# Kernel tuning notes

Hardware: AMD Instinct MI355X
Metric: run time of the kernel (lower is better)

The kernel has to match this reference:

```python
import jax, jax.numpy as jnp
import numpy as np

B, T, E, V, L, BLK = 2, 2048, 1024, 32000, 12, 2048


def setup_inputs() -> dict:
    key = jax.random.key(0)
    ks = jax.random.split(key, 10)
    std = 0.005  # FHE-friendly tiny init, matches nn.init.normal_(std=0.005)
    init = lambda k, shape: jax.random.normal(k, shape, jnp.float32) * std
    return {
        "idx": jax.random.randint(ks[0], (B, T), 0, V, dtype=jnp.int32),
        "wte": init(ks[1], (V, E)),
        "wpe": init(ks[2], (BLK, E)),
        "ln1_w": jnp.ones((L, E), jnp.float32),   # FHELayerNorm weights init to ones
        "Wq": init(ks[3], (L, E, E)),
        "Wk": init(ks[4], (L, E, E)),
        "Wv": init(ks[5], (L, E, E)),
        "Wo": init(ks[6], (L, E, E)),
        "ln2_w": jnp.ones((L, E), jnp.float32),
        "fc1": init(ks[7], (L, 2 * E, E)),
        "fc2": init(ks[8], (L, E, 2 * E)),
        "lnf_w": jnp.ones((E,), jnp.float32),
        "lm_head": init(ks[9], (V, E)),
    }


def reference(idx, wte, wpe, ln1_w, Wq, Wk, Wv, Wo, ln2_w, fc1, fc2, lnf_w, lm_head):
    t = idx.shape[1]
    # embeddings, each scaled by 0.01
    x = wte[idx] * 0.01 + (wpe[:t] * 0.01)[None, :, :]  # [B,T,E]

    n_layer = ln1_w.shape[0]
    # inter-block rescale: 0.1 after every block except the last
    scales = jnp.where(jnp.arange(n_layer) < n_layer - 1, 0.1, 1.0).astype(x.dtype)

    def block(x, p):
        ln1, wq, wk, wv, wo, ln2, f1, f2, s = p
        # FHELayerNorm: pure scaling
        h = x * ln1 * 0.1
        # attention (single head over full E, softmax-free quadratic weights)
        q = jnp.einsum('bte,fe->btf', h, wq) * 0.01
        k = jnp.einsum('bte,fe->btf', h, wk) * 0.01
        v = jnp.einsum('bte,fe->btf', h, wv) * 0.1
        a = jnp.einsum('btf,bsf->bts', q, k) * 0.01      # [B,T,T]
        a = a * a * 0.1 + a * 0.1                         # pointwise quadratic
        ao = jnp.einsum('bts,bsf->btf', a, v) * 0.01
        attn_out = jnp.einsum('btf,ef->bte', ao, wo) * 0.1
        x = (x * 0.5 + attn_out * 0.5) * 0.1
        # MLP with polynomial activation
        h2 = x * ln2 * 0.1
        m = jnp.einsum('bte,fe->btf', h2, f1) * 0.05      # [B,T,2E]
        m = m * m * 0.1 + m * 0.1
        m = jnp.einsum('btf,ef->bte', m, f2) * 0.05
        x = (x * 0.5 + m * 0.5) * 0.1
        return x * s, None

    x, _ = jax.lax.scan(block, x, (ln1_w, Wq, Wk, Wv, Wo, ln2_w, fc1, fc2, scales))
    x = x * lnf_w * 0.1  # final FHELayerNorm
    logits = jnp.einsum('bte,ve->btv', x, lm_head) * 0.5
    return logits
```

## Files before the change

kernel.cpp:

```cpp
#include <hip/hip_runtime.h>
#include <hip/hip_fp8.h>
#include <stdint.h>
#include <math.h>

typedef unsigned short u16;
typedef __attribute__((ext_vector_type(4))) short s16x4;
typedef __attribute__((ext_vector_type(4))) float f32x4;
typedef __attribute__((ext_vector_type(2))) long long llx2;

typedef __attribute__((address_space(1))) const uint32_t gas_u32;
typedef __attribute__((address_space(3))) uint32_t las_u32;

__device__ __forceinline__ u16 f2b(float f) {
  union { float f; uint32_t u; } v; v.f = f;
  uint32_t r = v.u + 0x7FFFu + ((v.u >> 16) & 1u);
  return (u16)(r >> 16);
}
__device__ __forceinline__ float b2f(u16 b) {
  union { uint32_t u; float f; } v; v.u = ((uint32_t)b) << 16; return v.f;
}
__device__ __forceinline__ uint8_t f8(float x) {
  __hip_fp8_e4m3 t(x);
  return (uint8_t)t.__x;
}
__device__ __forceinline__ int ipos(int k) {
  return (k & ~63) | (k & 7) | ((k & 32) >> 2) | ((k & 24) << 1);
}

__device__ __forceinline__ void gl_lds16(const void* g, void* l) {
  __builtin_amdgcn_global_load_lds((gas_u32*)g, (las_u32*)l, 16, 0, 0);
}
__device__ __forceinline__ void barrier_raw() {
  asm volatile("" ::: "memory");
  __builtin_amdgcn_s_barrier();
  asm volatile("" ::: "memory");
}

#define MM8(A_, B_, C_) __builtin_amdgcn_mfma_f32_16x16x32_fp8_fp8(A_, B_, C_, 0, 0, 0)

#define PHASE_MID() do { \
  asm volatile("s_waitcnt lgkmcnt(0)" ::: "memory"); \
  __builtin_amdgcn_sched_barrier(0); \
  __builtin_amdgcn_s_setprio(1); \
} while (0)
#define PHASE_END() do { \
  __builtin_amdgcn_s_setprio(0); \
  __builtin_amdgcn_sched_barrier(0); \
  barrier_raw(); \
} while (0)

__device__ __forceinline__ void xcd_swz(int nwg, int orig, int gx, int& bx, int& by) {
  const int xcd = orig & 7, rem = orig >> 3;
  const int qq = nwg >> 3, rr = nwg & 7;
  const int wg = (xcd < rr ? xcd * (qq + 1) : rr * (qq + 1) + (xcd - rr) * qq) + rem;
  bx = wg % gx; by = wg / gx;
}

struct GP8 {
  const uint8_t* A; long long asb;
  const uint8_t* B[3]; long long bsb;
  uint8_t* O[3]; long long osb;
  int K, lda, ldb, ldo;
  float m1[3], m2[3];
  int epi[3];
  int nsel, msel, nfirst;
  float qc;
  u16* xres; const float* lnw; float rscale; float oscale;
  uint8_t* h8out;
  float* fout; int ldf;
};

#define EPI_FRAG() do { \
  if (epi == 0) { \
    _Pragma("unroll") \
    for (int r = 0; r < 4; ++r) { \
      float y = (v[r] * m1v) * m2v; \
      Op[(size_t)(rbase + r) * p.ldo + ipos(col)] = f8(y); \
    } \
  } else if (epi == 1) { \
    const int b = rbase >> 11, rb = rbase & 2047; \
    uint32_t pk = 0; \
    _Pragma("unroll") \
    for (int r = 0; r < 4; ++r) { \
      float y = (v[r] * m1v) * m2v; \
      pk |= (uint32_t)f8(y) << (8 * r); \
    } \
    *(uint32_t*)(Op + (size_t)b * 2097152 + (size_t)col * 2048 + ipos(rb)) = pk; \
  } else if (epi == 2) { \
    _Pragma("unroll") \
    for (int r = 0; r < 4; ++r) { \
      float u = (v[r] * m1v) * m2v; \
      Op[(size_t)(rbase + r) * p.ldo + ipos(col)] = f8(u * u * p.qc + u); \
    } \
  } else if (epi == 3) { \
    _Pragma("unroll") \
    for (int r = 0; r < 4; ++r) { \
      float add = (v[r] * m1v) * m2v; \
      size_t ix = (size_t)(rbase + r) * 1024 + col; \
      float xn = (b2f(p.xres[ix]) + add) * p.rscale; \
      p.xres[ix] = f2b(xn); \
      float hv = xn * p.lnw[col] * 0.1f; \
      p.h8out[(size_t)(rbase + r) * 1024 + ipos(col)] = f8(hv * p.oscale); \
    } \
  } else { \
    _Pragma("unroll") \
    for (int r = 0; r < 4; ++r) \
      __builtin_nontemporal_store((v[r] * m1v) * m2v, \
                                  &p.fout[(size_t)(rbase + r) * p.ldf + col]); \
  } \
} while (0)

#define S8A(q, kh, t) do { \
  gl_lds16(gA0 + (size_t)(t) * 128 + (kh) * 64, lAw + (q) * 32768 + (kh) * 8192); \
  gl_lds16(gA1 + (size_t)(t) * 128 + (kh) * 64, lAw + (q) * 32768 + (kh) * 8192 + 4096); \
} while (0)
#define S8B(q, kh, t) do { \
  gl_lds16(gB0 + (size_t)(t) * 128 + (kh) * 64, lBw + (q) * 32768 + (kh) * 8192); \
  gl_lds16(gB1 + (size_t)(t) * 128 + (kh) * 64, lBw + (q) * 32768 + (kh) * 8192 + 4096); \
} while (0)

#define MF8() do { \
  acc[0][0]=MM8(a0[0],b0[0],acc[0][0]); acc[0][0]=MM8(a0[1],b0[1],acc[0][0]); \
  acc[0][1]=MM8(a0[0],b1[0],acc[0][1]); acc[0][1]=MM8(a0[1],b1[1],acc[0][1]); \
  acc[0][2]=MM8(a0[0],b2[0],acc[0][2]); acc[0][2]=MM8(a0[1],b2[1],acc[0][2]); \
  acc[0][3]=MM8(a0[0],b3[0],acc[0][3]); acc[0][3]=MM8(a0[1],b3[1],acc[0][3]); \
  acc[1][0]=MM8(a1[0],b0[0],acc[1][0]); acc[1][0]=MM8(a1[1],b0[1],acc[1][0]); \
  acc[1][1]=MM8(a1[0],b1[0],acc[1][1]); acc[1][1]=MM8(a1[1],b1[1],acc[1][1]); \
  acc[1][2]=MM8(a1[0],b2[0],acc[1][2]); acc[1][2]=MM8(a1[1],b2[1],acc[1][2]); \
  acc[1][3]=MM8(a1[0],b3[0],acc[1][3]); acc[1][3]=MM8(a1[1],b3[1],acc[1][3]); \
  acc[2][0]=MM8(a2[0],b0[0],acc[2][0]); acc[2][0]=MM8(a2[1],b0[1],acc[2][0]); \
  acc[2][1]=MM8(a2[0],b1[0],acc[2][1]); acc[2][1]=MM8(a2[1],b1[1],acc[2][1]); \
  acc[2][2]=MM8(a2[0],b2[0],acc[2][2]); acc[2][2]=MM8(a2[1],b2[1],acc[2][2]); \
  acc[2][3]=MM8(a2[0],b3[0],acc[2][3]); acc[2][3]=MM8(a2[1],b3[1],acc[2][3]); \
  acc[3][0]=MM8(a3[0],b0[0],acc[3][0]); acc[3][0]=MM8(a3[1],b0[1],acc[3][0]); \
  acc[3][1]=MM8(a3[0],b1[0],acc[3][1]); acc[3][1]=MM8(a3[1],b1[1],acc[3][1]); \
  acc[3][2]=MM8(a3[0],b2[0],acc[3][2]); acc[3][2]=MM8(a3[1],b2[1],acc[3][2]); \
  acc[3][3]=MM8(a3[0],b3[0],acc[3][3]); acc[3][3]=MM8(a3[1],b3[1],acc[3][3]); \
} while (0)

__global__ __launch_bounds__(256, 2) void gemm8_k(GP8 p) {
  extern __shared__ __attribute__((aligned(16))) char lds[];
  const int z = blockIdx.z;
  int bx, by;
  xcd_swz(gridDim.x * gridDim.y, blockIdx.y * gridDim.x + blockIdx.x, gridDim.x, bx, by);
  const int m0 = p.nfirst ? by * 128 : bx * 128;
  const int n0 = p.nfirst ? bx * 128 : by * 128;
  const int zi = p.nsel ? (n0 >> 10) : 0;
  const int nB = p.nsel ? (n0 & 1023) : n0;
  const uint8_t* __restrict__ Ap = p.A + (size_t)z * p.asb;
  const uint8_t* __restrict__ Bp = p.B[zi] + (size_t)(p.msel ? (m0 >> 11) : z) * p.bsb;

  const int tid = threadIdx.x, wid = tid >> 6, lane = tid & 63;
  const int wm = wid >> 1, wn = wid & 1;
  const int l15 = lane & 15, l4 = lane >> 4;
  const int cswz16 = (l4 ^ ((l15 >> 1) & 3)) * 16;

  const f32x4 vzero = {0.f, 0.f, 0.f, 0.f};
  f32x4 acc[4][4];
#pragma unroll
  for (int i = 0; i < 4; ++i)
#pragma unroll
    for (int j = 0; j < 4; ++j) acc[i][j] = vzero;

  const int sr = lane >> 2;
  const int cgB = ((lane & 3) ^ ((lane >> 3) & 3)) * 16;
  const uint8_t* gA0 = Ap + (size_t)(m0 + wid * 16 + sr) * p.lda + cgB;
  const uint8_t* gA1 = gA0 + (size_t)64 * p.lda;
  const uint8_t* gB0 = Bp + (size_t)(nB + wid * 16 + sr) * p.ldb + cgB;
  const uint8_t* gB1 = gB0 + (size_t)64 * p.ldb;
  char* lAw = lds + wid * 1024;
  char* lBw = lds + 16384 + wid * 1024;

  const int nt = p.K >> 7;

  S8A(0, 0, 0); S8B(0, 0, 0); S8A(0, 1, 0); S8B(0, 1, 0);
  S8A(1, 0, 1); S8B(1, 0, 1);
  asm volatile("s_waitcnt vmcnt(4)" ::: "memory");
  barrier_raw();

  llx2 a0, a1, a2, a3, b0, b1, b2, b3;
  for (int t = 0; t < nt; ++t) {
    const int q = t & 1;
    const char* Abase = lds + q * 32768 + (wm * 64 + l15) * 64 + cswz16;
    const char* Bbase = lds + q * 32768 + 16384 + (wn * 64 + l15) * 64 + cswz16;
    a0 = *(const llx2*)Abase;          a1 = *(const llx2*)(Abase + 1024);
    a2 = *(const llx2*)(Abase + 2048); a3 = *(const llx2*)(Abase + 3072);
    b0 = *(const llx2*)Bbase;          b1 = *(const llx2*)(Bbase + 1024);
    b2 = *(const llx2*)(Bbase + 2048); b3 = *(const llx2*)(Bbase + 3072);
    if (t + 1 < nt) { S8A(q ^ 1, 1, t + 1); S8B(q ^ 1, 1, t + 1); }
    PHASE_MID(); MF8(); PHASE_END();
    a0 = *(const llx2*)(Abase + 8192);        a1 = *(const llx2*)(Abase + 8192 + 1024);
    a2 = *(const llx2*)(Abase + 8192 + 2048); a3 = *(const llx2*)(Abase + 8192 + 3072);
    b0 = *(const llx2*)(Bbase + 8192);        b1 = *(const llx2*)(Bbase + 8192 + 1024);
    b2 = *(const llx2*)(Bbase + 8192 + 2048); b3 = *(const llx2*)(Bbase + 8192 + 3072);
    if (t + 2 < nt) { S8A(q, 0, t + 2); S8B(q, 0, t + 2); }
    PHASE_MID(); MF8();
    __builtin_amdgcn_s_setprio(0);
    __builtin_amdgcn_sched_barrier(0);
    if (t + 2 < nt) asm volatile("s_waitcnt vmcnt(4)" ::: "memory");
    else            asm volatile("s_waitcnt vmcnt(0)" ::: "memory");
    barrier_raw();
  }

  const int epi = p.epi[zi];
  const float m1v = p.m1[zi], m2v = p.m2[zi];
  uint8_t* __restrict__ Op = p.O[zi] + (size_t)z * p.osb;
#pragma unroll
  for (int mi = 0; mi < 4; ++mi) {
    const int rbase = m0 + wm * 64 + mi * 16 + l4 * 4;
#pragma unroll
    for (int ni = 0; ni < 4; ++ni) {
      const int col = nB + wn * 64 + ni * 16 + l15;
      f32x4 v = acc[mi][ni];
      EPI_FRAG();
    }
  }
}

#define H8STAGE(b, t) do { \
  gl_lds16(gA0 + (size_t)(t) * 128,      lds + (b) * 24576 + wid * 1024); \
  gl_lds16(gB0 + (size_t)(t) * 128,      lds + (b) * 24576 + 8192 + wid * 1024); \
  gl_lds16(gB1 + (size_t)(t) * 128,      lds + (b) * 24576 + 12288 + wid * 1024); \
  gl_lds16(gA0 + (size_t)(t) * 128 + 64, lds + (b) * 24576 + 4096 + wid * 1024); \
  gl_lds16(gB0 + (size_t)(t) * 128 + 64, lds + (b) * 24576 + 16384 + wid * 1024); \
  gl_lds16(gB1 + (size_t)(t) * 128 + 64, lds + (b) * 24576 + 20480 + wid * 1024); \
} while (0)

#define MF8H(AK, BK_) do { \
  acc[0][0]=MM8(a0##AK[0],b0##BK_[0],acc[0][0]); acc[0][0]=MM8(a0##AK[1],b0##BK_[1],acc[0][0]); \
  acc[0][1]=MM8(a0##AK[0],b1##BK_[0],acc[0][1]); acc[0][1]=MM8(a0##AK[1],b1##BK_[1],acc[0][1]); \
  acc[0][2]=MM8(a0##AK[0],b2##BK_[0],acc[0][2]); acc[0][2]=MM8(a0##AK[1],b2##BK_[1],acc[0][2]); \
  acc[0][3]=MM8(a0##AK[0],b3##BK_[0],acc[0][3]); acc[0][3]=MM8(a0##AK[1],b3##BK_[1],acc[0][3]); \
  acc[1][0]=MM8(a1##AK[0],b0##BK_[0],acc[1][0]); acc[1][0]=MM8(a1##AK[1],b0##BK_[1],acc[1][0]); \
  acc[1][1]=MM8(a1##AK[0],b1##BK_[0],acc[1][1]); acc[1][1]=MM8(a1##AK[1],b1##BK_[1],acc[1][1]); \
  acc[1][2]=MM8(a1##AK[0],b2##BK_[0],acc[1][2]); acc[1][2]=MM8(a1##AK[1],b2##BK_[1],acc[1][2]); \
  acc[1][3]=MM8(a1##AK[0],b3##BK_[0],acc[1][3]); acc[1][3]=MM8(a1##AK[1],b3##BK_[1],acc[1][3]); \
} while (0)

__global__ __launch_bounds__(256, 2) void gemm8h_k(GP8 p) {
  extern __shared__ __attribute__((aligned(16))) char lds[];
  const int z = blockIdx.z;
  int bx, by;
  xcd_swz(gridDim.x * gridDim.y, blockIdx.y * gridDim.x + blockIdx.x, gridDim.x, bx, by);
  const int m0 = bx * 64, n0 = by * 128;
  const int zi = p.nsel ? (n0 >> 10) : 0;
  const int nB = p.nsel ? (n0 & 1023) : n0;
  const uint8_t* __restrict__ Ap = p.A + (size_t)z * p.asb;
  const uint8_t* __restrict__ Bp = p.B[zi] + (size_t)(p.msel ? (m0 >> 11) : z) * p.bsb;

  const int tid = threadIdx.x, wid = tid >> 6, lane = tid & 63;
  const int wm = wid >> 1, wn = wid & 1;
  const int l15 = lane & 15, l4 = lane >> 4;
  const int cswz16 = (l4 ^ ((l15 >> 1) & 3)) * 16;

  const f32x4 vzero = {0.f, 0.f, 0.f, 0.f};
  f32x4 acc[2][4];
#pragma unroll
  for (int i = 0; i < 2; ++i)
#pragma unroll
    for (int j = 0; j < 4; ++j) acc[i][j] = vzero;

  const int sr = lane >> 2;
  const int cgB = ((lane & 3) ^ ((lane >> 3) & 3)) * 16;
  const uint8_t* gA0 = Ap + (size_t)(m0 + wid * 16 + sr) * p.lda + cgB;
  const uint8_t* gB0 = Bp + (size_t)(nB + wid * 16 + sr) * p.ldb + cgB;
  const uint8_t* gB1 = gB0 + (size_t)64 * p.ldb;

  const int nt = p.K >> 7;

  H8STAGE(0, 0);
  H8STAGE(1, 1);
  asm volatile("s_waitcnt vmcnt(6)" ::: "memory");
  barrier_raw();

  int q = 0;
  for (int t = 0; t < nt; ++t) {
    const int bn = (q == 0) ? 2 : q - 1;
    const char* Abase = lds + q * 24576 + (wm * 32 + l15) * 64 + cswz16;
    const char* Bbase = lds + q * 24576 + 8192 + (wn * 64 + l15) * 64 + cswz16;
    llx2 a0k0 = *(const llx2*)Abase;
    llx2 a1k0 = *(const llx2*)(Abase + 1024);
    llx2 a0k1 = *(const llx2*)(Abase + 4096);
    llx2 a1k1 = *(const llx2*)(Abase + 4096 + 1024);
    llx2 b0k0 = *(const llx2*)Bbase;
    llx2 b1k0 = *(const llx2*)(Bbase + 1024);
    llx2 b2k0 = *(const llx2*)(Bbase + 2048);
    llx2 b3k0 = *(const llx2*)(Bbase + 3072);
    llx2 b0k1 = *(const llx2*)(Bbase + 8192);
    llx2 b1k1 = *(const llx2*)(Bbase + 8192 + 1024);
    llx2 b2k1 = *(const llx2*)(Bbase + 8192 + 2048);
    llx2 b3k1 = *(const llx2*)(Bbase + 8192 + 3072);
    if (t + 2 < nt) H8STAGE(bn, t + 2);
    asm volatile("s_waitcnt lgkmcnt(0)" ::: "memory");
    __builtin_amdgcn_sched_barrier(0);
    __builtin_amdgcn_s_setprio(1);
    MF8H(k0, k0);
    MF8H(k1, k1);
    __builtin_amdgcn_s_setprio(0);
    __builtin_amdgcn_sched_barrier(0);
    if (t + 2 < nt) asm volatile("s_waitcnt vmcnt(6)" ::: "memory");
    else            asm volatile("s_waitcnt vmcnt(0)" ::: "memory");
    barrier_raw();
    q = (q == 2) ? 0 : q + 1;
  }

  const int epi = p.epi[zi];
  const float m1v = p.m1[zi], m2v = p.m2[zi];
  uint8_t* __restrict__ Op = p.O[zi] + (size_t)z * p.osb;
#pragma unroll
  for (int mi = 0; mi < 2; ++mi) {
    const int rbase = m0 + wm * 32 + mi * 16 + l4 * 4;
#pragma unroll
    for (int ni = 0; ni < 4; ++ni) {
      const int col = nB + wn * 64 + ni * 16 + l15;
      f32x4 v = acc[mi][ni];
      EPI_FRAG();
    }
  }
}

#define P8SA(b, t) do { \
  gl_lds16(gA0 + (size_t)(t) * 64,              lds + (b) * 24576 + wid * 1024); \
  gl_lds16(gA0 + (size_t)(t) * 64 + arow64,     lds + (b) * 24576 + 4096 + wid * 1024); \
  gl_lds16(gA0 + (size_t)(t) * 64 + 2 * arow64, lds + (b) * 24576 + 8192 + wid * 1024); \
  gl_lds16(gA0 + (size_t)(t) * 64 + 3 * arow64, lds + (b) * 24576 + 12288 + wid * 1024); \
} while (0)
#define P8SB(b, t) do { \
  gl_lds16(gB0 + (size_t)(t) * 64,          lds + (b) * 24576 + 16384 + wid * 1024); \
  gl_lds16(gB0 + (size_t)(t) * 64 + brow64, lds + (b) * 24576 + 20480 + wid * 1024); \
} while (0)

__global__ __launch_bounds__(256, 2) void gemm8p_k(GP8 p) {
  extern __shared__ __attribute__((aligned(16))) char lds[];
  const int z = blockIdx.z;
  int bx, by;
  xcd_swz(gridDim.x * gridDim.y, blockIdx.y * gridDim.x + blockIdx.x, gridDim.x, bx, by);
  const int n0 = bx * 128, m0 = by * 256;
  const int zi = 0;
  const uint8_t* __restrict__ Ap = p.A;
  const uint8_t* __restrict__ Bp = p.B[0];

  const int tid = threadIdx.x, wid = tid >> 6, lane = tid & 63;
  const int wm = wid >> 1, wn = wid & 1;
  const int l15 = lane & 15, l4 = lane >> 4;
  const int cswz16 = (l4 ^ ((l15 >> 1) & 3)) * 16;

  const f32x4 vzero = {0.f, 0.f, 0.f, 0.f};
  f32x4 acc[8][4];
#pragma unroll
  for (int i = 0; i < 8; ++i)
#pragma unroll
    for (int j = 0; j < 4; ++j) acc[i][j] = vzero;

  const int sr = lane >> 2;
  const int cgB = ((lane & 3) ^ ((lane >> 3) & 3)) * 16;
  const uint8_t* gA0 = Ap + (size_t)(m0 + wid * 16 + sr) * p.lda + cgB;
  const uint8_t* gB0 = Bp + (size_t)(n0 + wid * 16 + sr) * p.ldb + cgB;
  const size_t arow64 = (size_t)64 * p.lda;
  const size_t brow64 = (size_t)64 * p.ldb;

  const int nt = p.K >> 6;

  P8SA(0, 0); P8SB(0, 0);
  P8SA(1, 1); P8SB(1, 1);
  asm volatile("s_waitcnt vmcnt(6)" ::: "memory");
  barrier_raw();

  int q = 0;
  for (int t = 0; t < nt; ++t) {
    const int bn = (q == 0) ? 2 : q - 1;
    const char* Abase = lds + q * 24576 + (wm * 128 + l15) * 64 + cswz16;
    const char* Bbase = lds + q * 24576 + 16384 + (wn * 64 + l15) * 64 + cswz16;
    llx2 av[8], bv[4];
#pragma unroll
    for (int mi = 0; mi < 8; ++mi) av[mi] = *(const llx2*)(Abase + mi * 1024);
#pragma unroll
    for (int ni = 0; ni < 4; ++ni) bv[ni] = *(const llx2*)(Bbase + ni * 1024);
    if (t + 2 < nt) { P8SA(bn, t + 2); P8SB(bn, t + 2); }
    asm volatile("s_waitcnt lgkmcnt(0)" ::: "memory");
    __builtin_amdgcn_sched_barrier(0);
    __builtin_amdgcn_s_setprio(1);
#pragma unroll
    for (int mi = 0; mi < 8; ++mi)
#pragma unroll
      for (int ni = 0; ni < 4; ++ni) {
        acc[mi][ni] = MM8(av[mi][0], bv[ni][0], acc[mi][ni]);
        acc[mi][ni] = MM8(av[mi][1], bv[ni][1], acc[mi][ni]);
      }
    __builtin_amdgcn_s_setprio(0);
    __builtin_amdgcn_sched_barrier(0);
    if (t + 2 < nt) asm volatile("s_waitcnt vmcnt(6)" ::: "memory");
    else            asm volatile("s_waitcnt vmcnt(0)" ::: "memory");
    barrier_raw();
    q = (q == 2) ? 0 : q + 1;
  }

  const int epi = p.epi[zi];
  const float m1v = p.m1[zi], m2v = p.m2[zi];
  uint8_t* __restrict__ Op = p.O[zi];
#pragma unroll
  for (int mi = 0; mi < 8; ++mi) {
    const int rbase = m0 + wm * 128 + mi * 16 + l4 * 4;
#pragma unroll
    for (int ni = 0; ni < 4; ++ni) {
      const int col = n0 + wn * 64 + ni * 16 + l15;
      f32x4 v = acc[mi][ni];
      EPI_FRAG();
    }
  }
}

__global__ __launch_bounds__(256) void embed8_k(const int* __restrict__ idx, const float* __restrict__ wte,
                                                const float* __restrict__ wpe, const float* __restrict__ ln1,
                                                u16* __restrict__ x, uint8_t* __restrict__ h8, float sh) {
  const int bt = blockIdx.x;
  const int t = bt & 2047;
  const int tok = idx[bt];
  const int e = threadIdx.x * 4;
  const float4 wv = *(const float4*)(wte + (size_t)tok * 1024 + e);
  const float4 pv = *(const float4*)(wpe + (size_t)t * 1024 + e);
  const float4 lv = *(const float4*)(ln1 + e);
  float4 xo;
  xo.x = (wv.x + pv.x) * 0.01f;
  xo.y = (wv.y + pv.y) * 0.01f;
  xo.z = (wv.z + pv.z) * 0.01f;
  xo.w = (wv.w + pv.w) * 0.01f;
  s16x4 xb;
  xb[0] = (short)f2b(xo.x); xb[1] = (short)f2b(xo.y);
  xb[2] = (short)f2b(xo.z); xb[3] = (short)f2b(xo.w);
  *(s16x4*)(x + (size_t)bt * 1024 + e) = xb;
  uint32_t pk = (uint32_t)f8(xo.x * lv.x * 0.1f * sh)
              | ((uint32_t)f8(xo.y * lv.y * 0.1f * sh) << 8)
              | ((uint32_t)f8(xo.z * lv.z * 0.1f * sh) << 16)
              | ((uint32_t)f8(xo.w * lv.w * 0.1f * sh) << 24);
  *(uint32_t*)(h8 + (size_t)bt * 1024 + ipos(e)) = pk;
}

__global__ __launch_bounds__(256) void cvtT8_k(const float* __restrict__ src, uint8_t* __restrict__ dst,
                                               float scale) {
  __shared__ float tl[64][68];
  const int z = blockIdx.z;
  const int c0 = blockIdx.x * 64, r0 = blockIdx.y * 64;
  const int tid = threadIdx.x;
  const float* s = src + (size_t)z * 1048576;
#pragma unroll
  for (int it = 0; it < 4; ++it) {
    const int r = it * 16 + (tid >> 4);
    const int c4 = (tid & 15) * 4;
    const float4 v = *(const float4*)(s + (size_t)(r0 + r) * 1024 + c0 + c4);
    tl[r][c4] = v.x; tl[r][c4 + 1] = v.y; tl[r][c4 + 2] = v.z; tl[r][c4 + 3] = v.w;
  }
  __syncthreads();
  const int c = tid >> 2;
  const int rr = (tid & 3) * 16;
  const int base = r0 + rr;
  const int O = (base & ~63) | ((base & 32) >> 2) | ((base & 16) << 1);
  uint8_t* d = dst + (size_t)z * 1048576 + (size_t)(c0 + c) * 1024 + O;
  uint32_t w0 = 0, w1 = 0, w2 = 0, w3 = 0;
#pragma unroll
  for (int j = 0; j < 4; ++j) w0 |= (uint32_t)f8(tl[rr + j][c] * scale) << (8 * j);
#pragma unroll
  for (int j = 0; j < 4; ++j) w1 |= (uint32_t)f8(tl[rr + 4 + j][c] * scale) << (8 * j);
#pragma unroll
  for (int j = 0; j < 4; ++j) w2 |= (uint32_t)f8(tl[rr + 8 + j][c] * scale) << (8 * j);
#pragma unroll
  for (int j = 0; j < 4; ++j) w3 |= (uint32_t)f8(tl[rr + 12 + j][c] * scale) << (8 * j);
  *(uint32_t*)d = w0;        *(uint32_t*)(d + 4) = w1;
  *(uint32_t*)(d + 16) = w2; *(uint32_t*)(d + 20) = w3;
}

__global__ __launch_bounds__(256) void cvtf8i_k(const float* __restrict__ src, uint8_t* __restrict__ dst,
                                                long long n, float scale) {
  long long i = ((long long)blockIdx.x * 256 + threadIdx.x) * 8;
  const long long stride = (long long)gridDim.x * 256 * 8;
  for (; i < n; i += stride) {
    const float4 a = *(const float4*)(src + i);
    const float4 b = *(const float4*)(src + i + 4);
    uint32_t lo = (uint32_t)f8(a.x * scale) | ((uint32_t)f8(a.y * scale) << 8)
                | ((uint32_t)f8(a.z * scale) << 16) | ((uint32_t)f8(a.w * scale) << 24);
    uint32_t hi = (uint32_t)f8(b.x * scale) | ((uint32_t)f8(b.y * scale) << 8)
                | ((uint32_t)f8(b.z * scale) << 16) | ((uint32_t)f8(b.w * scale) << 24);
    uint8_t* d = dst + ((i & ~63ll) | (((i >> 3) & 3) << 4) | (((i >> 5) & 1) << 3));
    *(uint32_t*)d = lo;
    *(uint32_t*)(d + 4) = hi;
  }
}

__global__ __launch_bounds__(256) void megacvt8_k(const float* __restrict__ wq, const float* __restrict__ wk,
                                                  const float* __restrict__ f1, const float* __restrict__ f2,
                                                  uint8_t* __restrict__ dst, float scale) {
  const long long M1 = 1ll << 20;
  const long long per = 6 * M1;
  const long long total = 12 * per;
  long long i = ((long long)blockIdx.x * 256 + threadIdx.x) * 8;
  const long long stride = (long long)gridDim.x * 256 * 8;
  for (; i < total; i += stride) {
    const long long l = i / per;
    const long long off = i - l * per;
    const float* s; long long so;
    if      (off < M1)     { s = wq; so = l * M1 + off; }
    else if (off < 2 * M1) { s = wk; so = l * M1 + off - M1; }
    else if (off < 4 * M1) { s = f1; so = l * 2 * M1 + off - 2 * M1; }
    else                   { s = f2; so = l * 2 * M1 + off - 4 * M1; }
    const float4 a = *(const float4*)(s + so);
    const float4 b = *(const float4*)(s + so + 4);
    uint32_t lo = (uint32_t)f8(a.x * scale) | ((uint32_t)f8(a.y * scale) << 8)
                | ((uint32_t)f8(a.z * scale) << 16) | ((uint32_t)f8(a.w * scale) << 24);
    uint32_t hi = (uint32_t)f8(b.x * scale) | ((uint32_t)f8(b.y * scale) << 8)
                | ((uint32_t)f8(b.z * scale) << 16) | ((uint32_t)f8(b.w * scale) << 24);
    uint8_t* d = dst + ((i & ~63ll) | (((i >> 3) & 3) << 4) | (((i >> 5) & 1) << 3));
    *(uint32_t*)d = lo;
    *(uint32_t*)(d + 4) = hi;
  }
}

static inline double scp(double sigma) {
  double e = round(log2(0.5 / sigma));
  if (e > 120.0) e = 120.0;
  if (e < -120.0) e = -120.0;
  return ldexp(1.0, (int)e);
}
static inline void split2(double v, float& a, float& b) {
  if (v == 0.0) { a = 0.f; b = 0.f; return; }
  int e; frexp(v, &e);
  int h = e / 2;
  a = (float)ldexp(1.0, h);
  b = (float)ldexp(v, -h);
}

extern "C" void kernel_launch(void* const* d_in, const int* in_sizes, int n_in,
                              void* d_out, int out_size, void* d_ws, size_t ws_size,
                              hipStream_t stream) {
  const int*   idx  = (const int*)  d_in[0];
  const float* wte  = (const float*)d_in[1];
  const float* wpe  = (const float*)d_in[2];
  const float* ln1w = (const float*)d_in[3];
  const float* Wq   = (const float*)d_in[4];
  const float* Wk   = (const float*)d_in[5];
  const float* Wv   = (const float*)d_in[6];
  const float* Wo   = (const float*)d_in[7];
  const float* ln2w = (const float*)d_in[8];
  const float* fc1  = (const float*)d_in[9];
  const float* fc2  = (const float*)d_in[10];
  const float* lnfw = (const float*)d_in[11];
  const float* lmh  = (const float*)d_in[12];
  float* out = (float*)d_out;

  double dSh1[12], dSqk[12], dSaq[12], dSu[12], dSh2[12], dSmq[12], dShF;
  {
    double sx = 7e-5;
    for (int l = 0; l < 12; ++l) {
      double sh1 = sx * 0.1;
      double sq  = sh1 * 0.005 * 32.0 * 0.01;
      double saq = 32.0 * sq * sq * 0.01 * 0.1;
      double su  = sh1 * 8e-4 * 32.0 * 0.1;
      double sx2 = sx * 0.05;
      double sh2 = sx2 * 0.1;
      double smq = sh2 * 0.005 * 32.0 * 0.05 * 0.1;
      dSh1[l] = scp(sh1); dSqk[l] = scp(sq); dSaq[l] = scp(saq);
      dSu[l] = scp(su); dSh2[l] = scp(sh2); dSmq[l] = scp(smq);
      sx = sx2 * 0.05 * (l < 11 ? 0.1 : 1.0);
    }
    dShF = scp(sx * 0.1);
  }
  const double SW = 128.0, SWVO = 512.0, SF = 128.0, SL = 128.0;

  char* w = (char*)d_ws;
  u16*     x    = (u16*)w;      w += (size_t)4096 * 1024 * 2;
  uint8_t* h8   = (uint8_t*)w;  w += (size_t)4096 * 1024;
  uint8_t* q8   = (uint8_t*)w;  w += (size_t)4096 * 1024;
  uint8_t* k8   = (uint8_t*)w;  w += (size_t)4096 * 1024;
  uint8_t* uT8  = (uint8_t*)w;  w += (size_t)2 * 1024 * 2048;
  uint8_t* a8   = (uint8_t*)w;  w += (size_t)2 * 2048 * 2048;
  uint8_t* mb8  = (uint8_t*)w;  w += (size_t)4096 * 2048;
  uint8_t* lw8  = (uint8_t*)w;  w += (size_t)12 * 6291456;
  uint8_t* wvo8 = (uint8_t*)w;  w += (size_t)12 * 1048576;
  uint8_t* lmh8 = q8;
  uint8_t* wvT8 = lw8;
  uint8_t* wo8  = lw8 + 25165824;

  const size_t SH8 = 65536, SHH = 73728;

  embed8_k<<<4096, 256, 0, stream>>>(idx, wte, wpe, ln1w, x, h8, (float)dSh1[0]);

  cvtT8_k<<<dim3(16, 16, 12), 256, 0, stream>>>(Wv, wvT8, (float)SW);
  cvtf8i_k<<<2048, 256, 0, stream>>>(Wo, wo8, 12ll * 1048576, (float)SW);
  {
    GP8 p{};
    p.A = wo8; p.asb = 1048576;
    p.B[0] = wvT8; p.bsb = 1048576;
    p.O[0] = wvo8; p.osb = 1048576;
    p.K = 1024; p.lda = 1024; p.ldb = 1024; p.ldo = 1024;
    split2(SWVO / (SW * SW), p.m1[0], p.m2[0]);
    p.epi[0] = 0;
    gemm8_k<<<dim3(8, 8, 12), 256, SH8, stream>>>(p);
  }
  megacvt8_k<<<2048, 256, 0, stream>>>(Wq, Wk, fc1, fc2, lw8, (float)SW);

  for (int l = 0; l < 12; ++l) {
    uint8_t* lwl = lw8 + (size_t)l * 6291456;
    {
      GP8 p{};
      p.A = h8; p.asb = 0;
      p.B[0] = lwl; p.B[1] = lwl + 1048576; p.B[2] = wvo8 + (size_t)l * 1048576; p.bsb = 0;
      p.O[0] = q8; p.O[1] = k8; p.O[2] = uT8; p.osb = 0;
      p.K = 1024; p.lda = 1024; p.ldb = 1024; p.ldo = 1024;
      split2(0.01 * dSqk[l] / (dSh1[l] * SW), p.m1[0], p.m2[0]);
      p.m1[1] = p.m1[0]; p.m2[1] = p.m2[0];
      split2(0.1 * dSu[l] / (dSh1[l] * SWVO), p.m1[2], p.m2[2]);
      p.epi[0] = 0; p.epi[1] = 0; p.epi[2] = 1;
      p.nsel = 1;
      gemm8_k<<<dim3(32, 24, 1), 256, SH8, stream>>>(p);
    }
    {
      GP8 p{};
      p.A = q8; p.asb = 2097152;
      p.B[0] = k8; p.bsb = 2097152;
      p.O[0] = a8; p.osb = 4194304;
      p.K = 1024; p.lda = 1024; p.ldb = 1024; p.ldo = 2048;
      split2(0.001 * dSaq[l] / (dSqk[l] * dSqk[l]), p.m1[0], p.m2[0]);
      p.qc = (float)(10.0 / dSaq[l]);
      p.epi[0] = 2;
      gemm8_k<<<dim3(16, 16, 2), 256, SH8, stream>>>(p);
    }
    {
      GP8 p{};
      p.A = a8; p.asb = 0;
      p.B[0] = uT8; p.bsb = 2097152; p.msel = 1;
      p.O[0] = a8; p.osb = 0;
      p.K = 2048; p.lda = 2048; p.ldb = 2048; p.ldo = 1024;
      split2(0.001 / (dSaq[l] * dSu[l]), p.m1[0], p.m2[0]);
      p.epi[0] = 3;
      p.xres = x; p.lnw = ln2w + (size_t)l * 1024; p.rscale = 0.05f;
      p.oscale = (float)dSh2[l]; p.h8out = h8;
      gemm8h_k<<<dim3(64, 8, 1), 256, SHH, stream>>>(p);
    }
    {
      GP8 p{};
      p.A = h8; p.asb = 0;
      p.B[0] = lwl + 2097152; p.bsb = 0;
      p.O[0] = mb8; p.osb = 0;
      p.K = 1024; p.lda = 1024; p.ldb = 1024; p.ldo = 2048;
      split2(0.005 * dSmq[l] / (dSh2[l] * SF), p.m1[0], p.m2[0]);
      p.qc = (float)(10.0 / dSmq[l]);
      p.epi[0] = 2;
      gemm8_k<<<dim3(32, 16, 1), 256, SH8, stream>>>(p);
    }
    {
      GP8 p{};
      p.A = mb8; p.asb = 0;
      p.B[0] = lwl + 4194304; p.bsb = 0;
      p.O[0] = mb8; p.osb = 0;
      p.K = 2048; p.lda = 2048; p.ldb = 2048; p.ldo = 1024;
      split2(0.05 / (dSmq[l] * SF), p.m1[0], p.m2[0]);
      p.epi[0] = 3;
      p.xres = x;
      p.rscale = (l < 11) ? 0.005f : 0.05f;
      if (l < 11) { p.lnw = ln1w + (size_t)(l + 1) * 1024; p.oscale = (float)dSh1[l + 1]; }
      else        { p.lnw = lnfw; p.oscale = (float)dShF; }
      p.h8out = h8;
      gemm8h_k<<<dim3(64, 8, 1), 256, SHH, stream>>>(p);
    }
  }

  cvtf8i_k<<<2048, 256, 0, stream>>>(lmh, lmh8, 32768000ll, (float)SL);
  {
    GP8 p{};
    p.A = h8; p.asb = 0;
    p.B[0] = lmh8; p.bsb = 0;
    p.O[0] = lmh8; p.osb = 0;
    p.K = 1024; p.lda = 1024; p.ldb = 1024; p.ldo = 0;
    split2(0.5 / (dShF * SL), p.m1[0], p.m2[0]);
    p.epi[0] = 4;
    p.fout = out; p.ldf = 32000;
    gemm8p_k<<<dim3(250, 16, 1), 256, SHH, stream>>>(p);
  }
}
```

Baseline: 1.871 ms.

## Replace two-stage GEMM with triple-buffered BK=64 kernels and 256-row QKV tiles

Drops the old double-buffered BK=128 gemm8_k and adds gemm8t_k, a 128x128 kernel with a three-stage BK=64 LDS ring (48KB) and launch bounds allowing three blocks per CU. The QKV projection now uses the generalized 256x128 triple-buffered gemm8p_k, with nsel/msel/z-stride support added, so each B tile is reused over twice as many rows. The smaller LDS footprint is meant to raise occupancy and latency hiding for the attention-score, fc1 and weight-fold GEMMs. The trade-off is a 128-accumulator register load in the QKV kernel and fewer QKV blocks (384 instead of 768) to fill the GPU.

```diff
diff --git a/kernel.cpp b/kernel.cpp
--- a/kernel.cpp
+++ b/kernel.cpp
@@ -37,17 +37,6 @@
 }
 
 #define MM8(A_, B_, C_) __builtin_amdgcn_mfma_f32_16x16x32_fp8_fp8(A_, B_, C_, 0, 0, 0)
-
-#define PHASE_MID() do { \
-  asm volatile("s_waitcnt lgkmcnt(0)" ::: "memory"); \
-  __builtin_amdgcn_sched_barrier(0); \
-  __builtin_amdgcn_s_setprio(1); \
-} while (0)
-#define PHASE_END() do { \
-  __builtin_amdgcn_s_setprio(0); \
-  __builtin_amdgcn_sched_barrier(0); \
-  barrier_raw(); \
-} while (0)
 
 __device__ __forceinline__ void xcd_swz(int nwg, int orig, int gx, int& bx, int& by) {
   const int xcd = orig & 7, rem = orig >> 3;
@@ -63,7 +52,7 @@
   int K, lda, ldb, ldo;
   float m1[3], m2[3];
   int epi[3];
-  int nsel, msel, nfirst;
+  int nsel, msel;
   float qc;
   u16* xres; const float* lnw; float rscale; float oscale;
   uint8_t* h8out;
@@ -110,41 +99,23 @@
   } \
 } while (0)
 
-#define S8A(q, kh, t) do { \
-  gl_lds16(gA0 + (size_t)(t) * 128 + (kh) * 64, lAw + (q) * 32768 + (kh) * 8192); \
-  gl_lds16(gA1 + (size_t)(t) * 128 + (kh) * 64, lAw + (q) * 32768 + (kh) * 8192 + 4096); \
+#define P8SA(b, t) do { \
+  gl_lds16(gA0 + (size_t)(t) * 64,              lds + (b) * 24576 + wid * 1024); \
+  gl_lds16(gA0 + (size_t)(t) * 64 + arow64,     lds + (b) * 24576 + 4096 + wid * 1024); \
+  gl_lds16(gA0 + (size_t)(t) * 64 + 2 * arow64, lds + (b) * 24576 + 8192 + wid * 1024); \
+  gl_lds16(gA0 + (size_t)(t) * 64 + 3 * arow64, lds + (b) * 24576 + 12288 + wid * 1024); \
 } while (0)
-#define S8B(q, kh, t) do { \
-  gl_lds16(gB0 + (size_t)(t) * 128 + (kh) * 64, lBw + (q) * 32768 + (kh) * 8192); \
-  gl_lds16(gB1 + (size_t)(t) * 128 + (kh) * 64, lBw + (q) * 32768 + (kh) * 8192 + 4096); \
+#define P8SB(b, t) do { \
+  gl_lds16(gB0 + (size_t)(t) * 64,          lds + (b) * 24576 + 16384 + wid * 1024); \
+  gl_lds16(gB0 + (size_t)(t) * 64 + brow64, lds + (b) * 24576 + 20480 + wid * 1024); \
 } while (0)
 
-#define MF8() do { \
-  acc[0][0]=MM8(a0[0],b0[0],acc[0][0]); acc[0][0]=MM8(a0[1],b0[1],acc[0][0]); \
-  acc[0][1]=MM8(a0[0],b1[0],acc[0][1]); acc[0][1]=MM8(a0[1],b1[1],acc[0][1]); \
-  acc[0][2]=MM8(a0[0],b2[0],acc[0][2]); acc[0][2]=MM8(a0[1],b2[1],acc[0][2]); \
-  acc[0][3]=MM8(a0[0],b3[0],acc[0][3]); acc[0][3]=MM8(a0[1],b3[1],acc[0][3]); \
-  acc[1][0]=MM8(a1[0],b0[0],acc[1][0]); acc[1][0]=MM8(a1[1],b0[1],acc[1][0]); \
-  acc[1][1]=MM8(a1[0],b1[0],acc[1][1]); acc[1][1]=MM8(a1[1],b1[1],acc[1][1]); \
-  acc[1][2]=MM8(a1[0],b2[0],acc[1][2]); acc[1][2]=MM8(a1[1],b2[1],acc[1][2]); \
-  acc[1][3]=MM8(a1[0],b3[0],acc[1][3]); acc[1][3]=MM8(a1[1],b3[1],acc[1][3]); \
-  acc[2][0]=MM8(a2[0],b0[0],acc[2][0]); acc[2][0]=MM8(a2[1],b0[1],acc[2][0]); \
-  acc[2][1]=MM8(a2[0],b1[0],acc[2][1]); acc[2][1]=MM8(a2[1],b1[1],acc[2][1]); \
-  acc[2][2]=MM8(a2[0],b2[0],acc[2][2]); acc[2][2]=MM8(a2[1],b2[1],acc[2][2]); \
-  acc[2][3]=MM8(a2[0],b3[0],acc[2][3]); acc[2][3]=MM8(a2[1],b3[1],acc[2][3]); \
-  acc[3][0]=MM8(a3[0],b0[0],acc[3][0]); acc[3][0]=MM8(a3[1],b0[1],acc[3][0]); \
-  acc[3][1]=MM8(a3[0],b1[0],acc[3][1]); acc[3][1]=MM8(a3[1],b1[1],acc[3][1]); \
-  acc[3][2]=MM8(a3[0],b2[0],acc[3][2]); acc[3][2]=MM8(a3[1],b2[1],acc[3][2]); \
-  acc[3][3]=MM8(a3[0],b3[0],acc[3][3]); acc[3][3]=MM8(a3[1],b3[1],acc[3][3]); \
-} while (0)
-
-__global__ __launch_bounds__(256, 2) void gemm8_k(GP8 p) {
+__global__ __launch_bounds__(256, 2) void gemm8p_k(GP8 p) {
   extern __shared__ __attribute__((aligned(16))) char lds[];
   const int z = blockIdx.z;
   int bx, by;
   xcd_swz(gridDim.x * gridDim.y, blockIdx.y * gridDim.x + blockIdx.x, gridDim.x, bx, by);
-  const int m0 = p.nfirst ? by * 128 : bx * 128;
-  const int n0 = p.nfirst ? bx * 128 : by * 128;
+  const int n0 = bx * 128, m0 = by * 256;
   const int zi = p.nsel ? (n0 >> 10) : 0;
   const int nB = p.nsel ? (n0 & 1023) : n0;
   const uint8_t* __restrict__ Ap = p.A + (size_t)z * p.asb;
@@ -156,50 +127,143 @@
   const int cswz16 = (l4 ^ ((l15 >> 1) & 3)) * 16;
 
   const f32x4 vzero = {0.f, 0.f, 0.f, 0.f};
-  f32x4 acc[4][4];
-#pragma unroll
-  for (int i = 0; i < 4; ++i)
+  f32x4 acc[8][4];
+#pragma unroll
+  for (int i = 0; i < 8; ++i)
 #pragma unroll
     for (int j = 0; j < 4; ++j) acc[i][j] = vzero;
 
   const int sr = lane >> 2;
   const int cgB = ((lane & 3) ^ ((lane >> 3) & 3)) * 16;
   const uint8_t* gA0 = Ap + (size_t)(m0 + wid * 16 + sr) * p.lda + cgB;
-  const uint8_t* gA1 = gA0 + (size_t)64 * p.lda;
   const uint8_t* gB0 = Bp + (size_t)(nB + wid * 16 + sr) * p.ldb + cgB;
-  const uint8_t* gB1 = gB0 + (size_t)64 * p.ldb;
-  char* lAw = lds + wid * 1024;
-  char* lBw = lds + 16384 + wid * 1024;
-
-  const int nt = p.K >> 7;
-
-  S8A(0, 0, 0); S8B(0, 0, 0); S8A(0, 1, 0); S8B(0, 1, 0);
-  S8A(1, 0, 1); S8B(1, 0, 1);
+  const size_t arow64 = (size_t)64 * p.lda;
+  const size_t brow64 = (size_t)64 * p.ldb;
+
+  const int nt = p.K >> 6;
+
+  P8SA(0, 0); P8SB(0, 0);
+  P8SA(1, 1); P8SB(1, 1);
+  asm volatile("s_waitcnt vmcnt(6)" ::: "memory");
+  barrier_raw();
+
+  int q = 0;
+  for (int t = 0; t < nt; ++t) {
+    const int bn = (q == 0) ? 2 : q - 1;
+    const char* Abase = lds + q * 24576 + (wm * 128 + l15) * 64 + cswz16;
+    const char* Bbase = lds + q * 24576 + 16384 + (wn * 64 + l15) * 64 + cswz16;
+    llx2 av[8], bv[4];
+#pragma unroll
+    for (int mi = 0; mi < 8; ++mi) av[mi] = *(const llx2*)(Abase + mi * 1024);
+#pragma unroll
+    for (int ni = 0; ni < 4; ++ni) bv[ni] = *(const llx2*)(Bbase + ni * 1024);
+    if (t + 2 < nt) { P8SA(bn, t + 2); P8SB(bn, t + 2); }
+    asm volatile("s_waitcnt lgkmcnt(0)" ::: "memory");
+    __builtin_amdgcn_sched_barrier(0);
+    __builtin_amdgcn_s_setprio(1);
+#pragma unroll
+    for (int mi = 0; mi < 8; ++mi)
+#pragma unroll
+      for (int ni = 0; ni < 4; ++ni) {
+        acc[mi][ni] = MM8(av[mi][0], bv[ni][0], acc[mi][ni]);
+        acc[mi][ni] = MM8(av[mi][1], bv[ni][1], acc[mi][ni]);
+      }
+    __builtin_amdgcn_s_setprio(0);
+    __builtin_amdgcn_sched_barrier(0);
+    if (t + 2 < nt) asm volatile("s_waitcnt vmcnt(6)" ::: "memory");
+    else            asm volatile("s_waitcnt vmcnt(0)" ::: "memory");
+    barrier_raw();
+    q = (q == 2) ? 0 : q + 1;
+  }
+
+  const int epi = p.epi[zi];
+  const float m1v = p.m1[zi], m2v = p.m2[zi];
+  uint8_t* __restrict__ Op = p.O[zi] + (size_t)z * p.osb;
+#pragma unroll
+  for (int mi = 0; mi < 8; ++mi) {
+    const int rbase = m0 + wm * 128 + mi * 16 + l4 * 4;
+#pragma unroll
+    for (int ni = 0; ni < 4; ++ni) {
+      const int col = nB + wn * 64 + ni * 16 + l15;
+      f32x4 v = acc[mi][ni];
+      EPI_FRAG();
+    }
+  }
+}
+
+#define T8SA(b, t) do { \
+  gl_lds16(gA0 + (size_t)(t) * 64,          lds + (b) * 16384 + wid * 1024); \
+  gl_lds16(gA0 + (size_t)(t) * 64 + arow64, lds + (b) * 16384 + 4096 + wid * 1024); \
+} while (0)
+#define T8SB(b, t) do { \
+  gl_lds16(gB0 + (size_t)(t) * 64,          lds + (b) * 16384 + 8192 + wid * 1024); \
+  gl_lds16(gB0 + (size_t)(t) * 64 + brow64, lds + (b) * 16384 + 12288 + wid * 1024); \
+} while (0)
+
+__global__ __launch_bounds__(256, 3) void gemm8t_k(GP8 p) {
+  extern __shared__ __attribute__((aligned(16))) char lds[];
+  const int z = blockIdx.z;
+  int bx, by;
+  xcd_swz(gridDim.x * gridDim.y, blockIdx.y * gridDim.x + blockIdx.x, gridDim.x, bx, by);
+  const int m0 = bx * 128, n0 = by * 128;
+  const int zi = p.nsel ? (n0 >> 10) : 0;
+  const int nB = p.nsel ? (n0 & 1023) : n0;
+  const uint8_t* __restrict__ Ap = p.A + (size_t)z * p.asb;
+  const uint8_t* __restrict__ Bp = p.B[zi] + (size_t)(p.msel ? (m0 >> 11) : z) * p.bsb;
+
+  const int tid = threadIdx.x, wid = tid >> 6, lane = tid & 63;
+  const int wm = wid >> 1, wn = wid & 1;
+  const int l15 = lane & 15, l4 = lane >> 4;
+  const int cswz16 = (l4 ^ ((l15 >> 1) & 3)) * 16;
+
+  const f32x4 vzero = {0.f, 0.f, 0.f, 0.f};
+  f32x4 acc[4][4];
+#pragma unroll
+  for (int i = 0; i < 4; ++i)
+#pragma unroll
+    for (int j = 0; j < 4; ++j) acc[i][j] = vzero;
+
+  const int sr = lane >> 2;
+  const int cgB = ((lane & 3) ^ ((lane >> 3) & 3)) * 16;
+  const uint8_t* gA0 = Ap + (size_t)(m0 + wid * 16 + sr) * p.lda + cgB;
+  const uint8_t* gB0 = Bp + (size_t)(nB + wid * 16 + sr) * p.ldb + cgB;
+  const size_t arow64 = (size_t)64 * p.lda;
+  const size_t brow64 = (size_t)64 * p.ldb;
+
+  const int nt = p.K >> 6;
+
+  T8SA(0, 0); T8SB(0, 0);
+  T8SA(1, 1); T8SB(1, 1);
   asm volatile("s_waitcnt vmcnt(4)" ::: "memory");
   barrier_raw();
 
-  llx2 a0, a1, a2, a3, b0, b1, b2, b3;
+  int q = 0;
   for (int t = 0; t < nt; ++t) {
-    const int q = t & 1;
-    const char* Abase = lds + q * 32768 + (wm * 64 + l15) * 64 + cswz16;
-    const char* Bbase = lds + q * 32768 + 16384 + (wn * 64 + l15) * 64 + cswz16;
-    a0 = *(const llx2*)Abase;          a1 = *(const llx2*)(Abase + 1024);
-    a2 = *(const llx2*)(Abase + 2048); a3 = *(const llx2*)(Abase + 3072);
-    b0 = *(const llx2*)Bbase;          b1 = *(const llx2*)(Bbase + 1024);
-    b2 = *(const llx2*)(Bbase + 2048); b3 = *(const llx2*)(Bbase + 3072);
-    if (t + 1 < nt) { S8A(q ^ 1, 1, t + 1); S8B(q ^ 1, 1, t + 1); }
-    PHASE_MID(); MF8(); PHASE_END();
-    a0 = *(const llx2*)(Abase + 8192);        a1 = *(const llx2*)(Abase + 8192 + 1024);
-    a2 = *(const llx2*)(Abase + 8192 + 2048); a3 = *(const llx2*)(Abase + 8192 + 3072);
-    b0 = *(const llx2*)(Bbase + 8192);        b1 = *(const llx2*)(Bbase + 8192 + 1024);
-    b2 = *(const llx2*)(Bbase + 8192 + 2048); b3 = *(const llx2*)(Bbase + 8192 + 3072);
-    if (t + 2 < nt) { S8A(q, 0, t + 2); S8B(q, 0, t + 2); }
-    PHASE_MID(); MF8();
+    const int bn = (q == 0) ? 2 : q - 1;
+    const char* Abase = lds + q * 16384 + (wm * 64 + l15) * 64 + cswz16;
+    const char* Bbase = lds + q * 16384 + 8192 + (wn * 64 + l15) * 64 + cswz16;
+    llx2 av[4], bv[4];
+#pragma unroll
+    for (int mi = 0; mi < 4; ++mi) av[mi] = *(const llx2*)(Abase + mi * 1024);
+#pragma unroll
+    for (int ni = 0; ni < 4; ++ni) bv[ni] = *(const llx2*)(Bbase + ni * 1024);
+    if (t + 2 < nt) { T8SA(bn, t + 2); T8SB(bn, t + 2); }
+    asm volatile("s_waitcnt lgkmcnt(0)" ::: "memory");
+    __builtin_amdgcn_sched_barrier(0);
+    __builtin_amdgcn_s_setprio(1);
+#pragma unroll
+    for (int mi = 0; mi < 4; ++mi)
+#pragma unroll
+      for (int ni = 0; ni < 4; ++ni) {
+        acc[mi][ni] = MM8(av[mi][0], bv[ni][0], acc[mi][ni]);
+        acc[mi][ni] = MM8(av[mi][1], bv[ni][1], acc[mi][ni]);
+      }
     __builtin_amdgcn_s_setprio(0);
     __builtin_amdgcn_sched_barrier(0);
     if (t + 2 < nt) asm volatile("s_waitcnt vmcnt(4)" ::: "memory");
     else            asm volatile("s_waitcnt vmcnt(0)" ::: "memory");
     barrier_raw();
+    q = (q == 2) ? 0 : q + 1;
   }
 
   const int epi = p.epi[zi];
@@ -319,97 +383,6 @@
   }
 }
 
-#define P8SA(b, t) do { \
-  gl_lds16(gA0 + (size_t)(t) * 64,              lds + (b) * 24576 + wid * 1024); \
-  gl_lds16(gA0 + (size_t)(t) * 64 + arow64,     lds + (b) * 24576 + 4096 + wid * 1024); \
-  gl_lds16(gA0 + (size_t)(t) * 64 + 2 * arow64, lds + (b) * 24576 + 8192 + wid * 1024); \
-  gl_lds16(gA0 + (size_t)(t) * 64 + 3 * arow64, lds + (b) * 24576 + 12288 + wid * 1024); \
-} while (0)
-#define P8SB(b, t) do { \
-  gl_lds16(gB0 + (size_t)(t) * 64,          lds + (b) * 24576 + 16384 + wid * 1024); \
-  gl_lds16(gB0 + (size_t)(t) * 64 + brow64, lds + (b) * 24576 + 20480 + wid * 1024); \
-} while (0)
-
-__global__ __launch_bounds__(256, 2) void gemm8p_k(GP8 p) {
-  extern __shared__ __attribute__((aligned(16))) char lds[];
-  const int z = blockIdx.z;
-  int bx, by;
-  xcd_swz(gridDim.x * gridDim.y, blockIdx.y * gridDim.x + blockIdx.x, gridDim.x, bx, by);
-  const int n0 = bx * 128, m0 = by * 256;
-  const int zi = 0;
-  const uint8_t* __restrict__ Ap = p.A;
-  const uint8_t* __restrict__ Bp = p.B[0];
-
-  const int tid = threadIdx.x, wid = tid >> 6, lane = tid & 63;
-  const int wm = wid >> 1, wn = wid & 1;
-  const int l15 = lane & 15, l4 = lane >> 4;
-  const int cswz16 = (l4 ^ ((l15 >> 1) & 3)) * 16;
-
-  const f32x4 vzero = {0.f, 0.f, 0.f, 0.f};
-  f32x4 acc[8][4];
-#pragma unroll
-  for (int i = 0; i < 8; ++i)
-#pragma unroll
-    for (int j = 0; j < 4; ++j) acc[i][j] = vzero;
-
-  const int sr = lane >> 2;
-  const int cgB = ((lane & 3) ^ ((lane >> 3) & 3)) * 16;
-  const uint8_t* gA0 = Ap + (size_t)(m0 + wid * 16 + sr) * p.lda + cgB;
-  const uint8_t* gB0 = Bp + (size_t)(n0 + wid * 16 + sr) * p.ldb + cgB;
-  const size_t arow64 = (size_t)64 * p.lda;
-  const size_t brow64 = (size_t)64 * p.ldb;
-
-  const int nt = p.K >> 6;
-
-  P8SA(0, 0); P8SB(0, 0);
-  P8SA(1, 1); P8SB(1, 1);
-  asm volatile("s_waitcnt vmcnt(6)" ::: "memory");
-  barrier_raw();
-
-  int q = 0;
-  for (int t = 0; t < nt; ++t) {
-    const int bn = (q == 0) ? 2 : q - 1;
-    const char* Abase = lds + q * 24576 + (wm * 128 + l15) * 64 + cswz16;
-    const char* Bbase = lds + q * 24576 + 16384 + (wn * 64 + l15) * 64 + cswz16;
-    llx2 av[8], bv[4];
-#pragma unroll
-    for (int mi = 0; mi < 8; ++mi) av[mi] = *(const llx2*)(Abase + mi * 1024);
-#pragma unroll
-    for (int ni = 0; ni < 4; ++ni) bv[ni] = *(const llx2*)(Bbase + ni * 1024);
-    if (t + 2 < nt) { P8SA(bn, t + 2); P8SB(bn, t + 2); }
-    asm volatile("s_waitcnt lgkmcnt(0)" ::: "memory");
-    __builtin_amdgcn_sched_barrier(0);
-    __builtin_amdgcn_s_setprio(1);
-#pragma unroll
-    for (int mi = 0; mi < 8; ++mi)
-#pragma unroll
-      for (int ni = 0; ni < 4; ++ni) {
-        acc[mi][ni] = MM8(av[mi][0], bv[ni][0], acc[mi][ni]);
-        acc[mi][ni] = MM8(av[mi][1], bv[ni][1], acc[mi][ni]);
-      }
-    __builtin_amdgcn_s_setprio(0);
-    __builtin_amdgcn_sched_barrier(0);
-    if (t + 2 < nt) asm volatile("s_waitcnt vmcnt(6)" ::: "memory");
-    else            asm volatile("s_waitcnt vmcnt(0)" ::: "memory");
-    barrier_raw();
-    q = (q == 2) ? 0 : q + 1;
-  }
-
-  const int epi = p.epi[zi];
-  const float m1v = p.m1[zi], m2v = p.m2[zi];
-  uint8_t* __restrict__ Op = p.O[zi];
-#pragma unroll
-  for (int mi = 0; mi < 8; ++mi) {
-    const int rbase = m0 + wm * 128 + mi * 16 + l4 * 4;
-#pragma unroll
-    for (int ni = 0; ni < 4; ++ni) {
-      const int col = n0 + wn * 64 + ni * 16 + l15;
-      f32x4 v = acc[mi][ni];
-      EPI_FRAG();
-    }
-  }
-}
-
 __global__ __launch_bounds__(256) void embed8_k(const int* __restrict__ idx, const float* __restrict__ wte,
                                                 const float* __restrict__ wpe, const float* __restrict__ ln1,
                                                 u16* __restrict__ x, uint8_t* __restrict__ h8, float sh) {
@@ -579,7 +552,7 @@
   uint8_t* wvT8 = lw8;
   uint8_t* wo8  = lw8 + 25165824;
 
-  const size_t SH8 = 65536, SHH = 73728;
+  const size_t SHP = 73728, SHT = 49152, SHH = 73728;
 
   embed8_k<<<4096, 256, 0, stream>>>(idx, wte, wpe, ln1w, x, h8, (float)dSh1[0]);
 
@@ -593,7 +566,7 @@
     p.K = 1024; p.lda = 1024; p.ldb = 1024; p.ldo = 1024;
     split2(SWVO / (SW * SW), p.m1[0], p.m2[0]);
     p.epi[0] = 0;
-    gemm8_k<<<dim3(8, 8, 12), 256, SH8, stream>>>(p);
+    gemm8t_k<<<dim3(8, 8, 12), 256, SHT, stream>>>(p);
   }
   megacvt8_k<<<2048, 256, 0, stream>>>(Wq, Wk, fc1, fc2, lw8, (float)SW);
 
@@ -610,7 +583,7 @@
       split2(0.1 * dSu[l] / (dSh1[l] * SWVO), p.m1[2], p.m2[2]);
       p.epi[0] = 0; p.epi[1] = 0; p.epi[2] = 1;
       p.nsel = 1;
-      gemm8_k<<<dim3(32, 24, 1), 256, SH8, stream>>>(p);
+      gemm8p_k<<<dim3(24, 16, 1), 256, SHP, stream>>>(p);
     }
     {
       GP8 p{};
@@ -621,7 +594,7 @@
       split2(0.001 * dSaq[l] / (dSqk[l] * dSqk[l]), p.m1[0], p.m2[0]);
       p.qc = (float)(10.0 / dSaq[l]);
       p.epi[0] = 2;
-      gemm8_k<<<dim3(16, 16, 2), 256, SH8, stream>>>(p);
+      gemm8t_k<<<dim3(16, 16, 2), 256, SHT, stream>>>(p);
     }
     {
       GP8 p{};
@@ -644,7 +617,7 @@
       split2(0.005 * dSmq[l] / (dSh2[l] * SF), p.m1[0], p.m2[0]);
       p.qc = (float)(10.0 / dSmq[l]);
       p.epi[0] = 2;
-      gemm8_k<<<dim3(32, 16, 1), 256, SH8, stream>>>(p);
+      gemm8t_k<<<dim3(32, 16, 1), 256, SHT, stream>>>(p);
     }
     {
       GP8 p{};
@@ -673,6 +646,6 @@
     split2(0.5 / (dShF * SL), p.m1[0], p.m2[0]);
     p.epi[0] = 4;
     p.fout = out; p.ldf = 32000;
-    gemm8p_k<<<dim3(250, 16, 1), 256, SHH, stream>>>(p);
-  }
-}
+    gemm8p_k<<<dim3(250, 16, 1), 256, SHP, stream>>>(p);
+  }
+}
```

Result: no change. 1.904 ms (+1.7%).
